# Optimization experiments

Hardware: AMD Instinct MI355X
Metric: run time of the kernel (lower is better)

Reference implementation:

```python
import jax, jax.numpy as jnp
import numpy as np
from jax import lax


def _b_mask(out_c, in_c, kh, kw):
    # MaskedConv2d mask_type='B' for a 1xK kernel: zero strictly right-of-center taps
    m = np.ones((out_c, in_c, kh, kw), dtype=np.float32)
    m[:, :, kh // 2:, kw // 2 + 1:] = 0
    m[:, :, kh // 2 + 1:, :] = 0
    return jnp.asarray(m)


def _conv(x, w, b):
    # NCHW 'same' conv, stride 1
    y = lax.conv_general_dilated(x, w, (1, 1), 'SAME',
                                 dimension_numbers=('NCHW', 'OIHW', 'NCHW'))
    return y + b[None, :, None, None]


def setup_inputs() -> dict:
    key = jax.random.key(0)
    ks = jax.random.split(key, 7)
    B, C_in, H, W = 32, 3, 64, 64
    HC = 128
    return {
        'x': jax.random.normal(ks[0], (B, C_in, H, W), jnp.float32),
        'W_is': jax.random.normal(ks[1], (4 * HC, C_in, 1, 3), jnp.float32) * 0.1,
        'b_is': jax.random.normal(ks[2], (4 * HC,), jnp.float32) * 0.1,
        'W_ss': jax.random.normal(ks[3], (4 * HC, HC, 1, 3), jnp.float32) * 0.1,
        'b_ss': jax.random.normal(ks[4], (4 * HC,), jnp.float32) * 0.1,
        'h0': jax.random.normal(ks[5], (1, HC, 1, W), jnp.float32) * 0.05,
        'c0': jax.random.normal(ks[6], (1, HC, 1, W), jnp.float32) * 0.05,
    }


def reference(x, W_is, b_is, W_ss, b_ss, h0, c0):
    B, _, H, W = x.shape
    HC = h0.shape[1]
    W_is_m = W_is * _b_mask(*W_is.shape)
    W_ss_m = W_ss * _b_mask(*W_ss.shape)

    # input-to-state projection for all rows at once: [B, 4*HC, H, W]
    x_proj = _conv(x, W_is_m, b_is)
    x_rows = jnp.moveaxis(x_proj, 2, 0)[:, :, :, None, :]  # [H, B, 4HC, 1, W]

    h_init = jnp.broadcast_to(h0, (B, HC, 1, W))
    c_init = jnp.broadcast_to(c0, (B, HC, 1, W))

    def step(carry, row_x):
        h_prev, c_prev = carry
        gates = jax.nn.sigmoid(row_x + _conv(h_prev, W_ss_m, b_ss))
        o, f, i, g = jnp.split(gates, 4, axis=1)
        c = f * c_prev + i * g
        h = o * jnp.tanh(c)
        return (h, c), h

    _, hs = lax.scan(step, (h_init, c_init), x_rows)  # hs: [H, B, HC, 1, W]
    hidden = jnp.moveaxis(hs[:, :, :, 0, :], 0, 2)  # [B, HC, H, W]
    return hidden
```

## Files before the change

### kernel.cpp

```cpp
#include <hip/hip_runtime.h>
#include <hip/hip_bf16.h>

typedef unsigned short u16;
typedef unsigned int u32;
typedef unsigned long long u64;
typedef short bf16x8 __attribute__((ext_vector_type(8)));
typedef float f32x4  __attribute__((ext_vector_type(4)));


__device__ __forceinline__ u16 f2b(float f) {
    return __builtin_bit_cast(u16, __float2bfloat16(f));
}
__device__ __forceinline__ float sigm(float x) {
    return __builtin_amdgcn_rcpf(1.0f + __expf(-x));
}
__device__ __forceinline__ float tanh_fast(float x) {
    return 1.0f - 2.0f * __builtin_amdgcn_rcpf(__expf(2.0f * x) + 1.0f);
}

#define LINE(kt, lane) (((kt) * 64 + (lane)) * 16)
#define BUFBYTES (9 * 64 * 16)

__global__ __launch_bounds__(512, 2) void rowlstm_mfma8(
    const float* __restrict__ x,   const float* __restrict__ Wis,
    const float* __restrict__ bis, const float* __restrict__ Wss,
    const float* __restrict__ bss, const float* __restrict__ h0,
    const float* __restrict__ c0,  float* __restrict__ out,
    char* halo)
{
    __shared__ __align__(16) char lds_buf[2 * BUFBYTES];
    __shared__ u16  lds_x[3 * 64 * 17];
    __shared__ float lds_bias[512];

    const int tid  = threadIdx.x;
    const int s    = blockIdx.x;
    const int b    = blockIdx.y;
    const int wid  = tid >> 6;
    const int lane = tid & 63;
    const int q    = lane >> 4;
    const int n    = lane & 15;
    const int wbase = s * 16;

    char* hs_my = halo + ((size_t)(b * 4 + s) * 64) * 256;
    char* hs_up = halo + ((size_t)(b * 4 + (s > 0 ? s - 1 : 0)) * 64) * 256;

    for (int i = tid; i < 1152; i += 512)
        *(uint4*)(lds_buf + i * 16) = make_uint4(0, 0, 0, 0);
    __syncthreads();

    lds_bias[tid] = bis[tid] + bss[tid];

    for (int i = tid; i < 3264; i += 512) {
        int cch = i / 1088, rem = i % 1088;
        int r = rem / 17, wl1 = rem % 17;
        int gw = wbase + wl1 - 1;
        lds_x[i] = (gw < 0) ? (u16)0
                 : f2b(x[(((size_t)b * 3 + cch) * 64 + r) * 64 + gw]);
    }

    bf16x8 afr[4][9];
    {
        #pragma unroll
        for (int g = 0; g < 4; ++g) {
            int oc = g * 128 + wid * 16 + n;
            #pragma unroll
            for (int kt = 0; kt < 8; ++kt) {
                bf16x8 a;
                #pragma unroll
                for (int jj = 0; jj < 4; ++jj) {
                    int ic = kt * 16 + q * 4 + jj;
                    float2 wp = *(const float2*)&Wss[(size_t)(oc * 128 + ic) * 3];
                    a[jj]     = (short)f2b(wp.y);
                    a[4 + jj] = (short)f2b(wp.x);
                }
                afr[g][kt] = a;
            }
            bf16x8 ax = {0, 0, 0, 0, 0, 0, 0, 0};
            if (q == 0) {
                #pragma unroll
                for (int cch = 0; cch < 3; ++cch) {
                    float2 wp = *(const float2*)&Wis[(size_t)(oc * 3 + cch) * 3];
                    ax[cch]     = (short)f2b(wp.y);
                    ax[4 + cch] = (short)f2b(wp.x);
                }
            }
            afr[g][8] = ax;
        }
    }

    float cst[4];
    {
        u16 hw[4];
        #pragma unroll
        for (int reg = 0; reg < 4; ++reg) {
            int hc = wid * 16 + q * 4 + reg;
            int wg = wbase + n;
            cst[reg] = c0[hc * 64 + wg];
            hw[reg] = f2b(h0[hc * 64 + wg]);
        }
        u64 d01 = (u64)((u32)hw[0] | ((u32)hw[1] << 16))
                | ((u64)((u32)hw[2] | ((u32)hw[3] << 16)) << 32);
        *(u64*)(lds_buf + LINE(wid, lane)) = d01;
        int wl = n + 1;
        if (wl < 16)
            *(u64*)(lds_buf + LINE(wid, q * 16 + wl) + 8) = d01;
    }
    if (s > 0 && tid < 32) {
        int ic0 = tid * 4;
        u64 v = (u64)((u32)f2b(h0[(ic0 + 0) * 64 + wbase - 1]) | ((u32)f2b(h0[(ic0 + 1) * 64 + wbase - 1]) << 16))
              | ((u64)((u32)f2b(h0[(ic0 + 2) * 64 + wbase - 1]) | ((u32)f2b(h0[(ic0 + 3) * 64 + wbase - 1]) << 16)) << 32);
        *(u64*)(lds_buf + LINE(tid >> 2, (tid & 3) * 16) + 8) = v;
    }
    if (tid < 16) {
        int nn = tid;
        u32 d0 = (u32)lds_x[0 * 1088 + 0 * 17 + nn + 1] | ((u32)lds_x[1 * 1088 + 0 * 17 + nn + 1] << 16);
        u32 d1 = (u32)lds_x[2 * 1088 + 0 * 17 + nn + 1];
        u32 d2 = (u32)lds_x[0 * 1088 + 0 * 17 + nn]     | ((u32)lds_x[1 * 1088 + 0 * 17 + nn] << 16);
        u32 d3 = (u32)lds_x[2 * 1088 + 0 * 17 + nn];
        *(uint4*)(lds_buf + LINE(8, nn)) = make_uint4(d0, d1, d2, d3);
    }
    __syncthreads();

    f32x4 bias_r[4];
    #pragma unroll
    for (int g = 0; g < 4; ++g) {
        int oc = g * 128 + wid * 16 + q * 4;
        bias_r[g][0] = lds_bias[oc + 0];
        bias_r[g][1] = lds_bias[oc + 1];
        bias_r[g][2] = lds_bias[oc + 2];
        bias_r[g][3] = lds_bias[oc + 3];
    }

    u64 hv = 0, hn = 0;
    const bool is_cons = (s > 0) && (tid < 32);
    if (is_cons)
        hv = __hip_atomic_load((const u64*)(hs_up + (size_t)tid * 8),
                               __ATOMIC_RELAXED, __HIP_MEMORY_SCOPE_AGENT);

    for (int r = 0; r < 64; ++r) {
        char* rbuf = lds_buf + (r & 1) * BUFBYTES;
        char* wbuf = lds_buf + ((r & 1) ^ 1) * BUFBYTES;

        if (is_cons && r < 62)
            hn = __hip_atomic_load((const u64*)(hs_up + (size_t)(r + 1) * 256 + tid * 8),
                                   __ATOMIC_RELAXED, __HIP_MEMORY_SCOPE_AGENT);

        if (r < 63 && tid >= 64 && tid < 80) {
            int nn = tid - 64, r1 = r + 1;
            u32 d0 = (u32)lds_x[0 * 1088 + r1 * 17 + nn + 1] | ((u32)lds_x[1 * 1088 + r1 * 17 + nn + 1] << 16);
            u32 d1 = (u32)lds_x[2 * 1088 + r1 * 17 + nn + 1];
            u32 d2 = (u32)lds_x[0 * 1088 + r1 * 17 + nn]     | ((u32)lds_x[1 * 1088 + r1 * 17 + nn] << 16);
            u32 d3 = (u32)lds_x[2 * 1088 + r1 * 17 + nn];
            *(uint4*)(wbuf + LINE(8, nn)) = make_uint4(d0, d1, d2, d3);
        }

        f32x4 acc[4];
        acc[0] = bias_r[0]; acc[1] = bias_r[1];
        acc[2] = bias_r[2]; acc[3] = bias_r[3];
        #pragma unroll
        for (int kt = 0; kt < 9; ++kt) {
            bf16x8 bv = *(const bf16x8*)(rbuf + LINE(kt, lane));
            acc[0] = __builtin_amdgcn_mfma_f32_16x16x32_bf16(afr[0][kt], bv, acc[0], 0, 0, 0);
            acc[1] = __builtin_amdgcn_mfma_f32_16x16x32_bf16(afr[1][kt], bv, acc[1], 0, 0, 0);
            acc[2] = __builtin_amdgcn_mfma_f32_16x16x32_bf16(afr[2][kt], bv, acc[2], 0, 0, 0);
            acc[3] = __builtin_amdgcn_mfma_f32_16x16x32_bf16(afr[3][kt], bv, acc[3], 0, 0, 0);
        }

        float hval[4]; u16 hw[4];
        #pragma unroll
        for (int reg = 0; reg < 4; ++reg) {
            float o  = sigm(acc[0][reg]);
            float f  = sigm(acc[1][reg]);
            float ii = sigm(acc[2][reg]);
            float gg = sigm(acc[3][reg]);
            float cn = f * cst[reg] + ii * gg;
            cst[reg] = cn;
            float h = o * tanh_fast(cn);
            hval[reg] = h;
            hw[reg] = f2b(h);
        }

        u64 d01 = (u64)((u32)hw[0] | ((u32)hw[1] << 16))
                | ((u64)((u32)hw[2] | ((u32)hw[3] << 16)) << 32);
        *(u64*)(wbuf + LINE(wid, lane)) = d01;
        int wl = n + 1;
        if (wl < 16) {
            *(u64*)(wbuf + LINE(wid, q * 16 + wl) + 8) = d01;
        } else if (s < 3 && r < 63) {
            __hip_atomic_store((u64*)(hs_my + (size_t)r * 256 + (wid * 4 + q) * 8),
                               ~d01, __ATOMIC_RELAXED, __HIP_MEMORY_SCOPE_AGENT);
        }

        #pragma unroll
        for (int reg = 0; reg < 4; ++reg) {
            int hc = wid * 16 + q * 4 + reg;
            out[(((size_t)(b * 128 + hc)) * 64 + r) * 64 + wbase + n] = hval[reg];
        }

        if (is_cons && r < 63) {
            while (hv == 0) {
                __builtin_amdgcn_s_sleep(1);
                hv = __hip_atomic_load((const u64*)(hs_up + (size_t)r * 256 + tid * 8),
                                       __ATOMIC_RELAXED, __HIP_MEMORY_SCOPE_AGENT);
            }
            *(u64*)(wbuf + LINE(tid >> 2, (tid & 3) * 16) + 8) = ~hv;
            hv = hn;
        }

        __builtin_amdgcn_sched_barrier(0);
        asm volatile("s_waitcnt lgkmcnt(0)\n\ts_barrier" ::: "memory");
        __builtin_amdgcn_sched_barrier(0);
    }
}

extern "C" void kernel_launch(void* const* d_in, const int* in_sizes, int n_in,
                              void* d_out, int out_size, void* d_ws, size_t ws_size,
                              hipStream_t stream)
{
    const float* x   = (const float*)d_in[0];
    const float* Wis = (const float*)d_in[1];
    const float* bis = (const float*)d_in[2];
    const float* Wss = (const float*)d_in[3];
    const float* bss = (const float*)d_in[4];
    const float* h0  = (const float*)d_in[5];
    const float* c0  = (const float*)d_in[6];
    float* out = (float*)d_out;

    hipMemsetAsync(d_ws, 0, (size_t)32 * 4 * 64 * 256, stream);
    rowlstm_mfma8<<<dim3(4, 32), 512, 0, stream>>>(
        x, Wis, bis, Wss, bss, h0, c0, out, (char*)d_ws);
}
```

Measured before the change: 205.5 us.

## Defer output stores, split MFMA accumulators, merge gate reciprocals, cap spin

Each row's output store is deferred to the start of the next iteration so its global write overlaps the next row's MFMA chain. The MFMA chain is split across two accumulator sets to shorten the dependency chain, and is wrapped in raised wave priority. The next-row x-tile staging now runs after the MFMAs. Gate math merges the input-gate and candidate sigmoids into one reciprocal, saving a reciprocal per element at a small rounding difference. The halo spin-wait gains an iteration cap, which could let a consumer read stale data if the cap is ever reached.

```diff
diff --git a/kernel.cpp b/kernel.cpp
--- a/kernel.cpp
+++ b/kernel.cpp
@@ -11,17 +11,12 @@
 __device__ __forceinline__ u16 f2b(float f) {
     return __builtin_bit_cast(u16, __float2bfloat16(f));
 }
-__device__ __forceinline__ float sigm(float x) {
-    return __builtin_amdgcn_rcpf(1.0f + __expf(-x));
-}
-__device__ __forceinline__ float tanh_fast(float x) {
-    return 1.0f - 2.0f * __builtin_amdgcn_rcpf(__expf(2.0f * x) + 1.0f);
-}
 
 #define LINE(kt, lane) (((kt) * 64 + (lane)) * 16)
 #define BUFBYTES (9 * 64 * 16)
-
-__global__ __launch_bounds__(512, 2) void rowlstm_mfma8(
+#define SPIN_CAP (1 << 16)
+
+__global__ __launch_bounds__(512, 2) void rowlstm_mfma11(
     const float* __restrict__ x,   const float* __restrict__ Wis,
     const float* __restrict__ bis, const float* __restrict__ Wss,
     const float* __restrict__ bss, const float* __restrict__ h0,
@@ -137,13 +132,48 @@
         hv = __hip_atomic_load((const u64*)(hs_up + (size_t)tid * 8),
                                __ATOMIC_RELAXED, __HIP_MEMORY_SCOPE_AGENT);
 
+    float ph[4];
+    const float* obase = out + (((size_t)(b * 128 + wid * 16 + q * 4)) * 64) * 64
+                       + wbase + n;
+
     for (int r = 0; r < 64; ++r) {
         char* rbuf = lds_buf + (r & 1) * BUFBYTES;
         char* wbuf = lds_buf + ((r & 1) ^ 1) * BUFBYTES;
 
+        if (r > 0) {
+            #pragma unroll
+            for (int reg = 0; reg < 4; ++reg)
+                ((float*)obase)[(size_t)reg * 4096 + (r - 1) * 64] = ph[reg];
+        }
+
         if (is_cons && r < 62)
             hn = __hip_atomic_load((const u64*)(hs_up + (size_t)(r + 1) * 256 + tid * 8),
                                    __ATOMIC_RELAXED, __HIP_MEMORY_SCOPE_AGENT);
+
+        f32x4 acc[4], acc2[4];
+        acc[0] = bias_r[0]; acc[1] = bias_r[1];
+        acc[2] = bias_r[2]; acc[3] = bias_r[3];
+        acc2[0] = (f32x4){0,0,0,0}; acc2[1] = (f32x4){0,0,0,0};
+        acc2[2] = (f32x4){0,0,0,0}; acc2[3] = (f32x4){0,0,0,0};
+        __builtin_amdgcn_s_setprio(1);
+        #pragma unroll
+        for (int kt = 0; kt < 9; ++kt) {
+            bf16x8 bv = *(const bf16x8*)(rbuf + LINE(kt, lane));
+            if (kt & 1) {
+                acc2[0] = __builtin_amdgcn_mfma_f32_16x16x32_bf16(afr[0][kt], bv, acc2[0], 0, 0, 0);
+                acc2[1] = __builtin_amdgcn_mfma_f32_16x16x32_bf16(afr[1][kt], bv, acc2[1], 0, 0, 0);
+                acc2[2] = __builtin_amdgcn_mfma_f32_16x16x32_bf16(afr[2][kt], bv, acc2[2], 0, 0, 0);
+                acc2[3] = __builtin_amdgcn_mfma_f32_16x16x32_bf16(afr[3][kt], bv, acc2[3], 0, 0, 0);
+            } else {
+                acc[0] = __builtin_amdgcn_mfma_f32_16x16x32_bf16(afr[0][kt], bv, acc[0], 0, 0, 0);
+                acc[1] = __builtin_amdgcn_mfma_f32_16x16x32_bf16(afr[1][kt], bv, acc[1], 0, 0, 0);
+                acc[2] = __builtin_amdgcn_mfma_f32_16x16x32_bf16(afr[2][kt], bv, acc[2], 0, 0, 0);
+                acc[3] = __builtin_amdgcn_mfma_f32_16x16x32_bf16(afr[3][kt], bv, acc[3], 0, 0, 0);
+            }
+        }
+        __builtin_amdgcn_s_setprio(0);
+        acc[0] += acc2[0]; acc[1] += acc2[1];
+        acc[2] += acc2[2]; acc[3] += acc2[3];
 
         if (r < 63 && tid >= 64 && tid < 80) {
             int nn = tid - 64, r1 = r + 1;
@@ -154,29 +184,23 @@
             *(uint4*)(wbuf + LINE(8, nn)) = make_uint4(d0, d1, d2, d3);
         }
 
-        f32x4 acc[4];
-        acc[0] = bias_r[0]; acc[1] = bias_r[1];
-        acc[2] = bias_r[2]; acc[3] = bias_r[3];
-        #pragma unroll
-        for (int kt = 0; kt < 9; ++kt) {
-            bf16x8 bv = *(const bf16x8*)(rbuf + LINE(kt, lane));
-            acc[0] = __builtin_amdgcn_mfma_f32_16x16x32_bf16(afr[0][kt], bv, acc[0], 0, 0, 0);
-            acc[1] = __builtin_amdgcn_mfma_f32_16x16x32_bf16(afr[1][kt], bv, acc[1], 0, 0, 0);
-            acc[2] = __builtin_amdgcn_mfma_f32_16x16x32_bf16(afr[2][kt], bv, acc[2], 0, 0, 0);
-            acc[3] = __builtin_amdgcn_mfma_f32_16x16x32_bf16(afr[3][kt], bv, acc[3], 0, 0, 0);
-        }
-
-        float hval[4]; u16 hw[4];
+        u16 hw[4];
         #pragma unroll
         for (int reg = 0; reg < 4; ++reg) {
-            float o  = sigm(acc[0][reg]);
-            float f  = sigm(acc[1][reg]);
-            float ii = sigm(acc[2][reg]);
-            float gg = sigm(acc[3][reg]);
-            float cn = f * cst[reg] + ii * gg;
+            float eo = __expf(-acc[0][reg]);
+            float ef = __expf(-acc[1][reg]);
+            float ei = __expf(-acc[2][reg]);
+            float eg = __expf(-acc[3][reg]);
+            float f_ = __builtin_amdgcn_rcpf(1.0f + ef);
+            float t  = 1.0f + ei;
+            float ig = __builtin_amdgcn_rcpf(t + eg * t);
+            float cn = f_ * cst[reg] + ig;
             cst[reg] = cn;
-            float h = o * tanh_fast(cn);
-            hval[reg] = h;
+            float o_ = __builtin_amdgcn_rcpf(1.0f + eo);
+            float e2 = __expf(2.0f * cn);
+            float th = 1.0f - 2.0f * __builtin_amdgcn_rcpf(e2 + 1.0f);
+            float h  = o_ * th;
+            ph[reg] = h;
             hw[reg] = f2b(h);
         }
 
@@ -191,17 +215,14 @@
                                ~d01, __ATOMIC_RELAXED, __HIP_MEMORY_SCOPE_AGENT);
         }
 
-        #pragma unroll
-        for (int reg = 0; reg < 4; ++reg) {
-            int hc = wid * 16 + q * 4 + reg;
-            out[(((size_t)(b * 128 + hc)) * 64 + r) * 64 + wbase + n] = hval[reg];
-        }
-
         if (is_cons && r < 63) {
-            while (hv == 0) {
-                __builtin_amdgcn_s_sleep(1);
-                hv = __hip_atomic_load((const u64*)(hs_up + (size_t)r * 256 + tid * 8),
-                                       __ATOMIC_RELAXED, __HIP_MEMORY_SCOPE_AGENT);
+            if (hv == 0) {
+                int guard = 0;
+                do {
+                    __builtin_amdgcn_s_sleep(1);
+                    hv = __hip_atomic_load((const u64*)(hs_up + (size_t)r * 256 + tid * 8),
+                                           __ATOMIC_RELAXED, __HIP_MEMORY_SCOPE_AGENT);
+                } while (hv == 0 && ++guard < SPIN_CAP);
             }
             *(u64*)(wbuf + LINE(tid >> 2, (tid & 3) * 16) + 8) = ~hv;
             hv = hn;
@@ -211,6 +232,10 @@
         asm volatile("s_waitcnt lgkmcnt(0)\n\ts_barrier" ::: "memory");
         __builtin_amdgcn_sched_barrier(0);
     }
+
+    #pragma unroll
+    for (int reg = 0; reg < 4; ++reg)
+        ((float*)obase)[(size_t)reg * 4096 + 63 * 64] = ph[reg];
 }
 
 extern "C" void kernel_launch(void* const* d_in, const int* in_sizes, int n_in,
@@ -227,6 +252,6 @@
     float* out = (float*)d_out;
 
     hipMemsetAsync(d_ws, 0, (size_t)32 * 4 * 64 * 256, stream);
-    rowlstm_mfma8<<<dim3(4, 32), 512, 0, stream>>>(
+    rowlstm_mfma11<<<dim3(4, 32), 512, 0, stream>>>(
         x, Wis, bis, Wss, bss, h0, c0, out, (char*)d_ws);
 }
```

After: 211.1 us. 1.03x slower.
